# Optimization experiments

Measured on AMD Instinct MI355X. Metric: run time of the kernel, lower is better.

## Reference

```python
import jax, jax.numpy as jnp
import numpy as np

N_NODES = 128
B = 2048
N = B * N_NODES          # 262144 total nodes
E_PER = 512
E = B * E_PER            # 1048576 edges
H = 64                   # hidden_dim == embedding_dim
EPS = 1e-5


def _layernorm(x, g, b):
    m = x.mean(-1, keepdims=True)
    v = ((x - m) ** 2).mean(-1, keepdims=True)
    return (x - m) * jax.lax.rsqrt(v + EPS) * g + b


def setup_inputs() -> dict:
    key = jax.random.key(0)
    ks = jax.random.split(key, 16)
    node_feature = jax.random.randint(ks[0], (N,), 0, N_NODES, dtype=jnp.int32)
    # edges stay within each graph's node block
    offs = (jnp.arange(E, dtype=jnp.int32) // E_PER) * N_NODES
    src = offs + jax.random.randint(ks[1], (E,), 0, N_NODES, dtype=jnp.int32)
    dst = offs + jax.random.randint(ks[2], (E,), 0, N_NODES, dtype=jnp.int32)
    edge_index = jnp.stack([src, dst], axis=1)          # [E, 2]
    batch_ptr = jnp.arange(B + 1, dtype=jnp.int32) * N_NODES
    s = 0.1
    f32 = jnp.float32
    return {
        'node_feature': node_feature,
        'edge_index': edge_index,
        'batch_ptr': batch_ptr,
        'emb': jax.random.normal(ks[3], (N_NODES, H), f32),
        'gcn_w': jax.random.normal(ks[4], (H, H), f32) * s,
        'gcn_b': jnp.zeros((H,), f32),
        'lin1_w': jax.random.normal(ks[5], (H, H), f32) * s,
        'lin1_b': jnp.zeros((H,), f32),
        'lin2_w': jax.random.normal(ks[6], (H, H), f32) * s,
        'lin2_b': jnp.zeros((H,), f32),
        'ln_g': jnp.ones((H,), f32),
        'ln_b': jnp.zeros((H,), f32),
        'ex_w1': jax.random.normal(ks[7], (H, H), f32) * s,
        'ex_b1': jnp.zeros((H,), f32),
        'ex_ln_g': jnp.ones((H,), f32),
        'ex_ln_b': jnp.zeros((H,), f32),
        'ex_w2': jax.random.normal(ks[8], (H, 1), f32) * s,
        'ex_b2': jnp.zeros((1,), f32),
    }


def _forward(node_feature, edge_index, batch_ptr, emb, gcn_w, gcn_b,
             lin1_w, lin1_b, lin2_w, lin2_b, ln_g, ln_b,
             ex_w1, ex_b1, ex_ln_g, ex_ln_b, ex_w2, ex_b2):
    x = emb[node_feature]                                # [N, H] embedding lookup
    # --- GCNConv (PyG gcn_norm: self-loops + symmetric normalization) ---
    loops = jnp.arange(N, dtype=edge_index.dtype)
    src = jnp.concatenate([edge_index[:, 0], loops])
    dst = jnp.concatenate([edge_index[:, 1], loops])
    deg = jax.ops.segment_sum(jnp.ones_like(dst, dtype=x.dtype), dst, N)
    dinv = jnp.where(deg > 0, jax.lax.rsqrt(deg), 0.0)
    norm = dinv[src] * dinv[dst]                         # [E+N]
    h = x @ gcn_w                                        # linear (no bias)
    h = jax.ops.segment_sum(norm[:, None] * h[src], dst, N) + gcn_b
    # --- Linear -> ReLU -> Linear, residual, LayerNorm ---
    h = jnp.maximum(h @ lin1_w + lin1_b, 0.0) @ lin2_w + lin2_b
    ef = _layernorm(h + x, ln_g, ln_b)                   # [N, H]
    # --- cumsum-based group mean over batch_ptr segments ---
    cs = jnp.concatenate([jnp.zeros((1, H), ef.dtype), jnp.cumsum(ef, axis=0)], 0)
    size = (batch_ptr[1:] - batch_ptr[:-1]).astype(ef.dtype)
    means = (cs[batch_ptr[1:]] - cs[batch_ptr[:-1]]) / size[:, None]   # [B, H]
    # --- exit MLP: Linear -> LayerNorm -> ReLU -> Linear ---
    exit_action = jnp.maximum(_layernorm(means @ ex_w1 + ex_b1, ex_ln_g, ex_ln_b), 0.0) @ ex_w2 + ex_b2  # [B, 1]
    # --- pairwise edge logits + triu/tril gather (directed) ---
    efb = ef.reshape(B, N_NODES, H)
    scores = jnp.einsum('bnf,bmf->bnm', efb, efb) / jnp.sqrt(jnp.asarray(H, ef.dtype))
    iu0, iu1 = np.triu_indices(N_NODES, 1)
    il0, il1 = np.tril_indices(N_NODES, -1)
    i0 = jnp.asarray(np.concatenate([iu0, il0]))
    i1 = jnp.asarray(np.concatenate([iu1, il1]))
    edge_actions = scores[:, i0, i1]                     # [B, n^2 - n]
    return jnp.concatenate([edge_actions, exit_action], axis=-1)


def reference(node_feature, edge_index, batch_ptr, emb, gcn_w, gcn_b,
              lin1_w, lin1_b, lin2_w, lin2_b, ln_g, ln_b,
              ex_w1, ex_b1, ex_ln_g, ex_ln_b, ex_w2, ex_b2):
    return _forward(node_feature, edge_index, batch_ptr, emb, gcn_w, gcn_b,
                    lin1_w, lin1_b, lin2_w, lin2_b, ln_g, ln_b,
                    ex_w1, ex_b1, ex_ln_g, ex_ln_b, ex_w2, ex_b2)
```

## Files before the change

kernel.cpp:

```cpp
#include <hip/hip_runtime.h>

typedef __bf16 bf16_t;
typedef __bf16 bf16x8 __attribute__((ext_vector_type(8)));
typedef float  f32x4  __attribute__((ext_vector_type(4)));

#define LDR 72

__device__ __forceinline__ float bflo(unsigned u){ return __uint_as_float(u << 16); }
__device__ __forceinline__ float bfhi(unsigned u){ return __uint_as_float(u & 0xffff0000u); }

#define WS_MAP_OFF 24576

__global__ void prep_kernel(const float* __restrict__ emb,
                            const float* __restrict__ gcn_w,
                            const float* __restrict__ lin1_w,
                            const float* __restrict__ lin2_w,
                            bf16_t* __restrict__ ws)
{
    int t = blockIdx.x * 256 + threadIdx.x;
    bf16_t* emb_bf = ws;
    bf16_t* hw_bf  = ws + 8192;
    bf16_t* w1T    = ws + 16384;
    bf16_t* w2T    = ws + 20480;

    emb_bf[t] = (bf16_t)emb[t];
    int i = t >> 6, j = t & 63;
    float s = 0.f;
    #pragma unroll 8
    for (int k = 0; k < 64; ++k) s += emb[i*64 + k] * gcn_w[k*64 + j];
    hw_bf[t] = (bf16_t)s;
    if (t < 4096){
        int jj = t >> 6, kk = t & 63;
        w1T[t] = (bf16_t)lin1_w[kk*64 + jj];
        w2T[t] = (bf16_t)lin2_w[kk*64 + jj];
    }

    if (blockIdx.x == 0){
        __shared__ bf16_t pA[16*32];
        __shared__ bf16_t pB[16*32];
        int tid = threadIdx.x;
        for (int c = tid; c < 512; c += 256){
            int r = c >> 5, k = c & 31;
            pA[c] = (bf16_t)((k == 0) ? (float)r : ((k == 1) ? 1.f : 0.f));
            pB[c] = (bf16_t)((k == 0) ? 1.f : ((k == 1) ? (float)(128*r) : 0.f));
        }
        __syncthreads();
        if (tid < 64){
            int l15 = tid & 15, lg = tid >> 4;
            bf16x8 a  = *reinterpret_cast<const bf16x8*>(&pA[l15*32 + lg*8]);
            bf16x8 bb = *reinterpret_cast<const bf16x8*>(&pB[l15*32 + lg*8]);
            f32x4 acc = (f32x4){0.f,0.f,0.f,0.f};
            acc = __builtin_amdgcn_mfma_f32_16x16x32_bf16(a, bb, acc, 0, 0, 0);
            int* map = (int*)(ws + WS_MAP_OFF);
            #pragma unroll
            for (int r = 0; r < 4; ++r){
                int iv = (int)(acc[r] + 0.5f);
                map[tid*4 + r] = (iv & 127) | ((iv >> 7) << 8);
            }
        }
    }
}

__global__ __launch_bounds__(256, 3) void fused_kernel(
    const int*   __restrict__ node_feature,
    const int*   __restrict__ edge_index,
    const float* __restrict__ gcn_b,
    const float* __restrict__ lin1_b,
    const float* __restrict__ lin2_b,
    const float* __restrict__ ln_g,
    const float* __restrict__ ln_b,
    const float* __restrict__ ex_w1,
    const float* __restrict__ ex_b1,
    const float* __restrict__ ex_ln_g,
    const float* __restrict__ ex_ln_b,
    const float* __restrict__ ex_w2,
    const float* __restrict__ ex_b2,
    const bf16_t* __restrict__ ws,
    float* __restrict__ out)
{
    __shared__ __align__(16) bf16_t bufB[128*LDR];
    __shared__ __align__(16) bf16_t bufC[128*LDR];
    __shared__ unsigned short s_edge[512];
    __shared__ unsigned char  s_adj[512];
    __shared__ int   s_cnt[128];
    __shared__ int   s_start[128];
    __shared__ int   s_cur[128];
    __shared__ float s_dinv[128];
    __shared__ int   s_nf[128];
    __shared__ float s_b[320];
    __shared__ float s_pm[256];
    __shared__ float s_means[64];

    const int tid  = threadIdx.x;
    const int b    = blockIdx.x;
    const int wid  = tid >> 6;
    const int lane = tid & 63;
    const int l15  = lane & 15;
    const int lg   = lane >> 4;
    const long obase = (long)b * 16257;

    const bf16_t* emb_bf = ws;
    const bf16_t* hw_bf  = ws + 8192;
    const bf16_t* w1T    = ws + 16384;
    const bf16_t* w2T    = ws + 20480;

    int mi[4], mj[4];
    {
        const int* map = (const int*)(ws + WS_MAP_OFF);
        #pragma unroll
        for (int r = 0; r < 4; ++r){
            int m = map[lane*4 + r];
            mi[r] = m & 255; mj[r] = m >> 8;
        }
    }

    if (tid < 128){ s_nf[tid] = node_feature[b*128 + tid]; s_cnt[tid] = 0; }
    else if (tid < 192){
        int j = tid - 128;
        s_b[j]       = gcn_b[j];
        s_b[64 + j]  = lin1_b[j];
        s_b[128 + j] = lin2_b[j];
        s_b[192 + j] = ln_g[j];
        s_b[256 + j] = ln_b[j];
    }
    __syncthreads();

    {
        const int2* ei = reinterpret_cast<const int2*>(edge_index) + b*512;
        #pragma unroll
        for (int e = tid; e < 512; e += 256){
            int2 sd = ei[e];
            int s = sd.x & 127, d = sd.y & 127;
            s_edge[e] = (unsigned short)((s << 8) | d);
            atomicAdd(&s_cnt[d], 1);
        }
    }
    #pragma unroll
    for (int c = tid; c < 1024; c += 256){
        int row = c >> 3, ch = c & 7;
        int nf = s_nf[row];
        uint4 vh = reinterpret_cast<const uint4*>(hw_bf + nf*64)[ch];
        reinterpret_cast<uint4*>(&bufB[row*LDR])[ch] = vh;
    }
    __syncthreads();

    if (tid < 128) s_dinv[tid] = rsqrtf((float)(s_cnt[tid] + 1));
    if (tid < 64){
        int a0 = s_cnt[2*tid], a1 = s_cnt[2*tid+1];
        int s = a0 + a1;
        #pragma unroll
        for (int d = 1; d < 64; d <<= 1){
            int v = __shfl_up(s, d);
            if (lane >= d) s += v;
        }
        int excl = s - (a0 + a1);
        s_start[2*tid]   = excl;      s_cur[2*tid]   = excl;
        s_start[2*tid+1] = excl + a0; s_cur[2*tid+1] = excl + a0;
    }
    __syncthreads();
    #pragma unroll
    for (int e = tid; e < 512; e += 256){
        unsigned short sd = s_edge[e];
        int s = sd >> 8, d = sd & 255;
        int pos = atomicAdd(&s_cur[d], 1);
        s_adj[pos] = (unsigned char)s;
    }
    __syncthreads();

    {
        const int n  = tid >> 1;
        const int f0 = (tid & 1) << 5;
        float inner[32];
        #pragma unroll
        for (int f = 0; f < 32; ++f) inner[f] = 0.f;
        const float dn = s_dinv[n];
        {
            const uint4* hv = reinterpret_cast<const uint4*>(&bufB[n*LDR + f0]);
            #pragma unroll
            for (int q = 0; q < 4; ++q){
                uint4 v = hv[q];
                inner[q*8+0] += dn * bflo(v.x); inner[q*8+1] += dn * bfhi(v.x);
                inner[q*8+2] += dn * bflo(v.y); inner[q*8+3] += dn * bfhi(v.y);
                inner[q*8+4] += dn * bflo(v.z); inner[q*8+5] += dn * bfhi(v.z);
                inner[q*8+6] += dn * bflo(v.w); inner[q*8+7] += dn * bfhi(v.w);
            }
        }
        const int st = s_start[n], cn = s_cnt[n];
        for (int k = 0; k < cn; ++k){
            int src = s_adj[st + k];
            float w = s_dinv[src];
            const uint4* hv = reinterpret_cast<const uint4*>(&bufB[src*LDR + f0]);
            #pragma unroll
            for (int q = 0; q < 4; ++q){
                uint4 v = hv[q];
                inner[q*8+0] += w * bflo(v.x); inner[q*8+1] += w * bfhi(v.x);
                inner[q*8+2] += w * bflo(v.y); inner[q*8+3] += w * bfhi(v.y);
                inner[q*8+4] += w * bflo(v.z); inner[q*8+5] += w * bfhi(v.z);
                inner[q*8+6] += w * bflo(v.w); inner[q*8+7] += w * bfhi(v.w);
            }
        }
        #pragma unroll
        for (int f = 0; f < 32; ++f)
            bufC[n*LDR + f0 + f] = (bf16_t)(dn * inner[f] + s_b[f0 + f]);
    }
    __syncthreads();

    {
        bf16x8 af[2][2];
        #pragma unroll
        for (int fm = 0; fm < 2; ++fm)
            #pragma unroll
            for (int kk = 0; kk < 2; ++kk)
                af[fm][kk] = *reinterpret_cast<const bf16x8*>(
                    &bufC[(wid*32 + fm*16 + l15)*LDR + kk*32 + lg*8]);
        f32x4 acc[2][4];
        #pragma unroll
        for (int fm = 0; fm < 2; ++fm)
            #pragma unroll
            for (int fn = 0; fn < 4; ++fn)
                acc[fm][fn] = (f32x4){0.f,0.f,0.f,0.f};
        #pragma unroll
        for (int fn = 0; fn < 4; ++fn){
            #pragma unroll
            for (int kk = 0; kk < 2; ++kk){
                bf16x8 bfr = *reinterpret_cast<const bf16x8*>(
                    &w1T[(fn*16 + l15)*64 + kk*32 + lg*8]);
                #pragma unroll
                for (int fm = 0; fm < 2; ++fm)
                    acc[fm][fn] = __builtin_amdgcn_mfma_f32_16x16x32_bf16(
                        af[fm][kk], bfr, acc[fm][fn], 0, 0, 0);
            }
        }
        #pragma unroll
        for (int fm = 0; fm < 2; ++fm)
            #pragma unroll
            for (int fn = 0; fn < 4; ++fn)
                #pragma unroll
                for (int r = 0; r < 4; ++r){
                    int row = wid*32 + fm*16 + mi[r];
                    int col = fn*16 + mj[r];
                    float v = acc[fm][fn][r] + s_b[64 + col];
                    bufB[row*LDR + col] = (bf16_t)fmaxf(v, 0.f);
                }
    }
    __syncthreads();

    {
        bf16x8 af[2][2];
        #pragma unroll
        for (int fm = 0; fm < 2; ++fm)
            #pragma unroll
            for (int kk = 0; kk < 2; ++kk)
                af[fm][kk] = *reinterpret_cast<const bf16x8*>(
                    &bufB[(wid*32 + fm*16 + l15)*LDR + kk*32 + lg*8]);
        f32x4 acc[2][4];
        #pragma unroll
        for (int fm = 0; fm < 2; ++fm)
            #pragma unroll
            for (int fn = 0; fn < 4; ++fn)
                acc[fm][fn] = (f32x4){0.f,0.f,0.f,0.f};
        #pragma unroll
        for (int fn = 0; fn < 4; ++fn){
            #pragma unroll
            for (int kk = 0; kk < 2; ++kk){
                bf16x8 bfr = *reinterpret_cast<const bf16x8*>(
                    &w2T[(fn*16 + l15)*64 + kk*32 + lg*8]);
                #pragma unroll
                for (int fm = 0; fm < 2; ++fm)
                    acc[fm][fn] = __builtin_amdgcn_mfma_f32_16x16x32_bf16(
                        af[fm][kk], bfr, acc[fm][fn], 0, 0, 0);
            }
        }
        #pragma unroll
        for (int fm = 0; fm < 2; ++fm)
            #pragma unroll
            for (int fn = 0; fn < 4; ++fn)
                #pragma unroll
                for (int r = 0; r < 4; ++r){
                    int row = wid*32 + fm*16 + mi[r];
                    int col = fn*16 + mj[r];
                    bufC[row*LDR + col] = (bf16_t)(acc[fm][fn][r] + s_b[128 + col]);
                }
    }
    __syncthreads();

    {
        const int n  = tid >> 1;
        const int f0 = (tid & 1) << 5;
        const bf16x8* xp = reinterpret_cast<const bf16x8*>(&emb_bf[s_nf[n]*64 + f0]);
        float vv[32];
        float p1 = 0.f, p2 = 0.f;
        const bf16x8* rp = reinterpret_cast<const bf16x8*>(&bufC[n*LDR + f0]);
        #pragma unroll
        for (int q = 0; q < 4; ++q){
            bf16x8 v8 = rp[q];
            bf16x8 x8 = xp[q];
            #pragma unroll
            for (int e = 0; e < 8; ++e){
                float f = (float)v8[e] + (float)x8[e];
                vv[q*8+e] = f; p1 += f; p2 += f*f;
            }
        }
        p1 += __shfl_xor(p1, 1);
        p2 += __shfl_xor(p2, 1);
        float mean = p1 * 0.015625f;
        float var  = p2 * 0.015625f - mean*mean;
        float rstd = rsqrtf(var + 1e-5f);
        #pragma unroll
        for (int j = 0; j < 32; ++j)
            bufC[n*LDR + f0 + j] =
                (bf16_t)((vv[j] - mean) * rstd * s_b[192 + f0 + j] + s_b[256 + f0 + j]);
    }
    __syncthreads();

    {
        int col = tid & 63, q = tid >> 6;
        float s = 0.f;
        #pragma unroll 8
        for (int r = q*32; r < q*32 + 32; ++r)
            s += (float)bufC[r*LDR + col];
        s_pm[q*64 + col] = s;
    }
    __syncthreads();
    if (tid < 64)
        s_means[tid] = (s_pm[tid] + s_pm[64+tid] + s_pm[128+tid] + s_pm[192+tid]) * 0.0078125f;
    __syncthreads();

    if (tid < 64){
        float a = ex_b1[lane];
        #pragma unroll 8
        for (int k = 0; k < 64; ++k)
            a += s_means[k] * ex_w1[k*64 + lane];
        float p1 = a, p2 = a*a;
        #pragma unroll
        for (int m = 1; m < 64; m <<= 1){ p1 += __shfl_xor(p1, m); p2 += __shfl_xor(p2, m); }
        float mean = p1 * 0.015625f;
        float var  = p2 * 0.015625f - mean*mean;
        float u = (a - mean) * rsqrtf(var + 1e-5f) * ex_ln_g[lane] + ex_ln_b[lane];
        u = fmaxf(u, 0.f);
        float prod = u * ex_w2[lane];
        #pragma unroll
        for (int m = 1; m < 64; m <<= 1) prod += __shfl_xor(prod, m);
        if (lane == 0) out[obase + 16256] = prod + ex_b2[0];
    }

    {
        bf16x8 af[2][2];
        #pragma unroll
        for (int fm = 0; fm < 2; ++fm)
            #pragma unroll
            for (int kk = 0; kk < 2; ++kk)
                af[fm][kk] = *reinterpret_cast<const bf16x8*>(
                    &bufC[(wid*32 + fm*16 + l15)*LDR + kk*32 + lg*8]);
        f32x4 acc[2][8];
        #pragma unroll
        for (int fm = 0; fm < 2; ++fm)
            #pragma unroll
            for (int fn = 0; fn < 8; ++fn)
                acc[fm][fn] = (f32x4){0.f,0.f,0.f,0.f};
        #pragma unroll
        for (int fn = 0; fn < 8; ++fn){
            #pragma unroll
            for (int kk = 0; kk < 2; ++kk){
                bf16x8 bfr = *reinterpret_cast<const bf16x8*>(
                    &bufC[(fn*16 + l15)*LDR + kk*32 + lg*8]);
                #pragma unroll
                for (int fm = 0; fm < 2; ++fm)
                    acc[fm][fn] = __builtin_amdgcn_mfma_f32_16x16x32_bf16(
                        af[fm][kk], bfr, acc[fm][fn], 0, 0, 0);
            }
        }
        float* ob = out + obase;
        #pragma unroll
        for (int fm = 0; fm < 2; ++fm){
            #pragma unroll
            for (int fn = 0; fn < 8; ++fn){
                #pragma unroll
                for (int r = 0; r < 4; ++r){
                    int i = wid*32 + fm*16 + mi[r];
                    int j = fn*16 + mj[r];
                    if (i != j){
                        float v = acc[fm][fn][r] * 0.125f;
                        int p = (i < j) ? (i*127 - ((i*(i-1)) >> 1) + j - i - 1)
                                        : (8128 + ((i*(i-1)) >> 1) + j);
                        ob[p] = v;
                    }
                }
            }
        }
    }
}

extern "C" void kernel_launch(void* const* d_in, const int* in_sizes, int n_in,
                              void* d_out, int out_size, void* d_ws, size_t ws_size,
                              hipStream_t stream)
{
    const int*   node_feature = (const int*)  d_in[0];
    const int*   edge_index   = (const int*)  d_in[1];
    const float* emb     = (const float*)d_in[3];
    const float* gcn_w   = (const float*)d_in[4];
    const float* gcn_b   = (const float*)d_in[5];
    const float* lin1_w  = (const float*)d_in[6];
    const float* lin1_b  = (const float*)d_in[7];
    const float* lin2_w  = (const float*)d_in[8];
    const float* lin2_b  = (const float*)d_in[9];
    const float* ln_g    = (const float*)d_in[10];
    const float* ln_b    = (const float*)d_in[11];
    const float* ex_w1   = (const float*)d_in[12];
    const float* ex_b1   = (const float*)d_in[13];
    const float* ex_ln_g = (const float*)d_in[14];
    const float* ex_ln_b = (const float*)d_in[15];
    const float* ex_w2   = (const float*)d_in[16];
    const float* ex_b2   = (const float*)d_in[17];
    bf16_t* ws  = (bf16_t*)d_ws;
    float*  out = (float*)d_out;

    prep_kernel<<<32, 256, 0, stream>>>(emb, gcn_w, lin1_w, lin2_w, ws);
    fused_kernel<<<2048, 256, 0, stream>>>(node_feature, edge_index,
        gcn_b, lin1_b, lin2_b, ln_g, ln_b,
        ex_w1, ex_b1, ex_ln_g, ex_ln_b, ex_w2, ex_b2,
        ws, out);
}
```

Before: 70.77 us.

## Double block threads to 512 and alias shared scratch into one pool

Raises the fused kernel block size from 256 to 512 threads, so each wave now owns 16 rows instead of 32 in every MFMA stage and four threads share a node in the aggregation and layernorm stages. Shared scratch arrays are overlaid in a single pool and the separate degree-count array is dropped, with counts derived from prefix-start differences. This is meant to add latency hiding and shrink per-thread register and LDS footprint. In exchange, each B fragment is reused across fewer MFMAs and there are more waves per barrier.

After: 80.35 us. 1.14x slower.

```diff
diff --git a/kernel.cpp b/kernel.cpp
--- a/kernel.cpp
+++ b/kernel.cpp
@@ -61,7 +61,7 @@
     }
 }
 
-__global__ __launch_bounds__(256, 3) void fused_kernel(
+__global__ __launch_bounds__(512, 6) void fused_kernel(
     const int*   __restrict__ node_feature,
     const int*   __restrict__ edge_index,
     const float* __restrict__ gcn_b,
@@ -80,16 +80,16 @@
 {
     __shared__ __align__(16) bf16_t bufB[128*LDR];
     __shared__ __align__(16) bf16_t bufC[128*LDR];
-    __shared__ unsigned short s_edge[512];
-    __shared__ unsigned char  s_adj[512];
-    __shared__ int   s_cnt[128];
-    __shared__ int   s_start[128];
-    __shared__ int   s_cur[128];
-    __shared__ float s_dinv[128];
+    __shared__ __align__(16) unsigned char pool[2112];
+    __shared__ float s_b[320];
     __shared__ int   s_nf[128];
-    __shared__ float s_b[320];
-    __shared__ float s_pm[256];
-    __shared__ float s_means[64];
+
+    unsigned char* s_adj   = pool;
+    int*           s_start = (int*)(pool + 512);
+    int*           s_cur   = (int*)(pool + 1040);
+    float*         s_dinv  = (float*)(pool + 1552);
+    float*         s_pm    = (float*)pool;
+    float*         s_means = (float*)(pool + 1024);
 
     const int tid  = threadIdx.x;
     const int b    = blockIdx.x;
@@ -114,7 +114,9 @@
         }
     }
 
-    if (tid < 128){ s_nf[tid] = node_feature[b*128 + tid]; s_cnt[tid] = 0; }
+    const int2* ei = reinterpret_cast<const int2*>(edge_index) + b*512;
+
+    if (tid < 128){ s_nf[tid] = node_feature[b*128 + tid]; s_cur[tid] = 0; }
     else if (tid < 192){
         int j = tid - 128;
         s_b[j]       = gcn_b[j];
@@ -126,27 +128,21 @@
     __syncthreads();
 
     {
-        const int2* ei = reinterpret_cast<const int2*>(edge_index) + b*512;
-        #pragma unroll
-        for (int e = tid; e < 512; e += 256){
-            int2 sd = ei[e];
-            int s = sd.x & 127, d = sd.y & 127;
-            s_edge[e] = (unsigned short)((s << 8) | d);
-            atomicAdd(&s_cnt[d], 1);
-        }
+        int2 sd = ei[tid];
+        atomicAdd(&s_cur[sd.y & 127], 1);
     }
     #pragma unroll
-    for (int c = tid; c < 1024; c += 256){
+    for (int c = tid; c < 1024; c += 512){
         int row = c >> 3, ch = c & 7;
-        int nf = s_nf[row];
-        uint4 vh = reinterpret_cast<const uint4*>(hw_bf + nf*64)[ch];
+        uint4 vh = reinterpret_cast<const uint4*>(hw_bf + s_nf[row]*64)[ch];
         reinterpret_cast<uint4*>(&bufB[row*LDR])[ch] = vh;
     }
     __syncthreads();
 
-    if (tid < 128) s_dinv[tid] = rsqrtf((float)(s_cnt[tid] + 1));
     if (tid < 64){
-        int a0 = s_cnt[2*tid], a1 = s_cnt[2*tid+1];
+        int a0 = s_cur[2*tid], a1 = s_cur[2*tid+1];
+        s_dinv[2*tid]   = rsqrtf((float)(a0 + 1));
+        s_dinv[2*tid+1] = rsqrtf((float)(a1 + 1));
         int s = a0 + a1;
         #pragma unroll
         for (int d = 1; d < 64; d <<= 1){
@@ -154,30 +150,32 @@
             if (lane >= d) s += v;
         }
         int excl = s - (a0 + a1);
-        s_start[2*tid]   = excl;      s_cur[2*tid]   = excl;
-        s_start[2*tid+1] = excl + a0; s_cur[2*tid+1] = excl + a0;
-    }
-    __syncthreads();
-    #pragma unroll
-    for (int e = tid; e < 512; e += 256){
-        unsigned short sd = s_edge[e];
-        int s = sd >> 8, d = sd & 255;
-        int pos = atomicAdd(&s_cur[d], 1);
-        s_adj[pos] = (unsigned char)s;
-    }
-    __syncthreads();
-
-    {
-        const int n  = tid >> 1;
-        const int f0 = (tid & 1) << 5;
-        float inner[32];
-        #pragma unroll
-        for (int f = 0; f < 32; ++f) inner[f] = 0.f;
+        s_start[2*tid]   = excl;
+        s_start[2*tid+1] = excl + a0;
+        if (tid == 63) s_start[128] = 512;
+        s_cur[2*tid]   = excl;
+        s_cur[2*tid+1] = excl + a0;
+    }
+    __syncthreads();
+
+    {
+        int2 sd = ei[tid];
+        int pos = atomicAdd(&s_cur[sd.y & 127], 1);
+        s_adj[pos] = (unsigned char)(sd.x & 127);
+    }
+    __syncthreads();
+
+    {
+        const int n  = tid >> 2;
+        const int f0 = (tid & 3) << 4;
+        float inner[16];
+        #pragma unroll
+        for (int f = 0; f < 16; ++f) inner[f] = 0.f;
         const float dn = s_dinv[n];
         {
             const uint4* hv = reinterpret_cast<const uint4*>(&bufB[n*LDR + f0]);
             #pragma unroll
-            for (int q = 0; q < 4; ++q){
+            for (int q = 0; q < 2; ++q){
                 uint4 v = hv[q];
                 inner[q*8+0] += dn * bflo(v.x); inner[q*8+1] += dn * bfhi(v.x);
                 inner[q*8+2] += dn * bflo(v.y); inner[q*8+3] += dn * bfhi(v.y);
@@ -185,13 +183,13 @@
                 inner[q*8+6] += dn * bflo(v.w); inner[q*8+7] += dn * bfhi(v.w);
             }
         }
-        const int st = s_start[n], cn = s_cnt[n];
+        const int st = s_start[n], cn = s_start[n+1] - st;
         for (int k = 0; k < cn; ++k){
             int src = s_adj[st + k];
             float w = s_dinv[src];
             const uint4* hv = reinterpret_cast<const uint4*>(&bufB[src*LDR + f0]);
             #pragma unroll
-            for (int q = 0; q < 4; ++q){
+            for (int q = 0; q < 2; ++q){
                 uint4 v = hv[q];
                 inner[q*8+0] += w * bflo(v.x); inner[q*8+1] += w * bfhi(v.x);
                 inner[q*8+2] += w * bflo(v.y); inner[q*8+3] += w * bfhi(v.y);
@@ -200,99 +198,76 @@
             }
         }
         #pragma unroll
-        for (int f = 0; f < 32; ++f)
+        for (int f = 0; f < 16; ++f)
             bufC[n*LDR + f0 + f] = (bf16_t)(dn * inner[f] + s_b[f0 + f]);
     }
     __syncthreads();
 
     {
-        bf16x8 af[2][2];
-        #pragma unroll
-        for (int fm = 0; fm < 2; ++fm)
-            #pragma unroll
-            for (int kk = 0; kk < 2; ++kk)
-                af[fm][kk] = *reinterpret_cast<const bf16x8*>(
-                    &bufC[(wid*32 + fm*16 + l15)*LDR + kk*32 + lg*8]);
-        f32x4 acc[2][4];
-        #pragma unroll
-        for (int fm = 0; fm < 2; ++fm)
-            #pragma unroll
-            for (int fn = 0; fn < 4; ++fn)
-                acc[fm][fn] = (f32x4){0.f,0.f,0.f,0.f};
-        #pragma unroll
-        for (int fn = 0; fn < 4; ++fn){
+        bf16x8 af[2];
+        #pragma unroll
+        for (int kk = 0; kk < 2; ++kk)
+            af[kk] = *reinterpret_cast<const bf16x8*>(
+                &bufC[(wid*16 + l15)*LDR + kk*32 + lg*8]);
+        f32x4 acc[4];
+        #pragma unroll
+        for (int fn = 0; fn < 4; ++fn) acc[fn] = (f32x4){0.f,0.f,0.f,0.f};
+        #pragma unroll
+        for (int fn = 0; fn < 4; ++fn)
             #pragma unroll
             for (int kk = 0; kk < 2; ++kk){
                 bf16x8 bfr = *reinterpret_cast<const bf16x8*>(
                     &w1T[(fn*16 + l15)*64 + kk*32 + lg*8]);
-                #pragma unroll
-                for (int fm = 0; fm < 2; ++fm)
-                    acc[fm][fn] = __builtin_amdgcn_mfma_f32_16x16x32_bf16(
-                        af[fm][kk], bfr, acc[fm][fn], 0, 0, 0);
-            }
-        }
-        #pragma unroll
-        for (int fm = 0; fm < 2; ++fm)
-            #pragma unroll
-            for (int fn = 0; fn < 4; ++fn)
-                #pragma unroll
-                for (int r = 0; r < 4; ++r){
-                    int row = wid*32 + fm*16 + mi[r];
-                    int col = fn*16 + mj[r];
-                    float v = acc[fm][fn][r] + s_b[64 + col];
-                    bufB[row*LDR + col] = (bf16_t)fmaxf(v, 0.f);
-                }
-    }
-    __syncthreads();
-
-    {
-        bf16x8 af[2][2];
-        #pragma unroll
-        for (int fm = 0; fm < 2; ++fm)
-            #pragma unroll
-            for (int kk = 0; kk < 2; ++kk)
-                af[fm][kk] = *reinterpret_cast<const bf16x8*>(
-                    &bufB[(wid*32 + fm*16 + l15)*LDR + kk*32 + lg*8]);
-        f32x4 acc[2][4];
-        #pragma unroll
-        for (int fm = 0; fm < 2; ++fm)
-            #pragma unroll
-            for (int fn = 0; fn < 4; ++fn)
-                acc[fm][fn] = (f32x4){0.f,0.f,0.f,0.f};
-        #pragma unroll
-        for (int fn = 0; fn < 4; ++fn){
+                acc[fn] = __builtin_amdgcn_mfma_f32_16x16x32_bf16(af[kk], bfr, acc[fn], 0, 0, 0);
+            }
+        #pragma unroll
+        for (int fn = 0; fn < 4; ++fn)
+            #pragma unroll
+            for (int r = 0; r < 4; ++r){
+                int row = wid*16 + mi[r];
+                int col = fn*16 + mj[r];
+                bufB[row*LDR + col] = (bf16_t)fmaxf(acc[fn][r] + s_b[64 + col], 0.f);
+            }
+    }
+    __syncthreads();
+
+    {
+        bf16x8 af[2];
+        #pragma unroll
+        for (int kk = 0; kk < 2; ++kk)
+            af[kk] = *reinterpret_cast<const bf16x8*>(
+                &bufB[(wid*16 + l15)*LDR + kk*32 + lg*8]);
+        f32x4 acc[4];
+        #pragma unroll
+        for (int fn = 0; fn < 4; ++fn) acc[fn] = (f32x4){0.f,0.f,0.f,0.f};
+        #pragma unroll
+        for (int fn = 0; fn < 4; ++fn)
             #pragma unroll
             for (int kk = 0; kk < 2; ++kk){
                 bf16x8 bfr = *reinterpret_cast<const bf16x8*>(
                     &w2T[(fn*16 + l15)*64 + kk*32 + lg*8]);
-                #pragma unroll
-                for (int fm = 0; fm < 2; ++fm)
-                    acc[fm][fn] = __builtin_amdgcn_mfma_f32_16x16x32_bf16(
-                        af[fm][kk], bfr, acc[fm][fn], 0, 0, 0);
-            }
-        }
-        #pragma unroll
-        for (int fm = 0; fm < 2; ++fm)
-            #pragma unroll
-            for (int fn = 0; fn < 4; ++fn)
-                #pragma unroll
-                for (int r = 0; r < 4; ++r){
-                    int row = wid*32 + fm*16 + mi[r];
-                    int col = fn*16 + mj[r];
-                    bufC[row*LDR + col] = (bf16_t)(acc[fm][fn][r] + s_b[128 + col]);
-                }
-    }
-    __syncthreads();
-
-    {
-        const int n  = tid >> 1;
-        const int f0 = (tid & 1) << 5;
+                acc[fn] = __builtin_amdgcn_mfma_f32_16x16x32_bf16(af[kk], bfr, acc[fn], 0, 0, 0);
+            }
+        #pragma unroll
+        for (int fn = 0; fn < 4; ++fn)
+            #pragma unroll
+            for (int r = 0; r < 4; ++r){
+                int row = wid*16 + mi[r];
+                int col = fn*16 + mj[r];
+                bufC[row*LDR + col] = (bf16_t)(acc[fn][r] + s_b[128 + col]);
+            }
+    }
+    __syncthreads();
+
+    {
+        const int n  = tid >> 2;
+        const int f0 = (tid & 3) << 4;
         const bf16x8* xp = reinterpret_cast<const bf16x8*>(&emb_bf[s_nf[n]*64 + f0]);
-        float vv[32];
+        const bf16x8* rp = reinterpret_cast<const bf16x8*>(&bufC[n*LDR + f0]);
+        float vv[16];
         float p1 = 0.f, p2 = 0.f;
-        const bf16x8* rp = reinterpret_cast<const bf16x8*>(&bufC[n*LDR + f0]);
-        #pragma unroll
-        for (int q = 0; q < 4; ++q){
+        #pragma unroll
+        for (int q = 0; q < 2; ++q){
             bf16x8 v8 = rp[q];
             bf16x8 x8 = xp[q];
             #pragma unroll
@@ -301,19 +276,19 @@
                 vv[q*8+e] = f; p1 += f; p2 += f*f;
             }
         }
-        p1 += __shfl_xor(p1, 1);
-        p2 += __shfl_xor(p2, 1);
+        p1 += __shfl_xor(p1, 1); p2 += __shfl_xor(p2, 1);
+        p1 += __shfl_xor(p1, 2); p2 += __shfl_xor(p2, 2);
         float mean = p1 * 0.015625f;
         float var  = p2 * 0.015625f - mean*mean;
         float rstd = rsqrtf(var + 1e-5f);
         #pragma unroll
-        for (int j = 0; j < 32; ++j)
+        for (int j = 0; j < 16; ++j)
             bufC[n*LDR + f0 + j] =
                 (bf16_t)((vv[j] - mean) * rstd * s_b[192 + f0 + j] + s_b[256 + f0 + j]);
     }
     __syncthreads();
 
-    {
+    if (tid < 256){
         int col = tid & 63, q = tid >> 6;
         float s = 0.f;
         #pragma unroll 8
@@ -345,46 +320,34 @@
     }
 
     {
-        bf16x8 af[2][2];
-        #pragma unroll
-        for (int fm = 0; fm < 2; ++fm)
-            #pragma unroll
-            for (int kk = 0; kk < 2; ++kk)
-                af[fm][kk] = *reinterpret_cast<const bf16x8*>(
-                    &bufC[(wid*32 + fm*16 + l15)*LDR + kk*32 + lg*8]);
-        f32x4 acc[2][8];
-        #pragma unroll
-        for (int fm = 0; fm < 2; ++fm)
-            #pragma unroll
-            for (int fn = 0; fn < 8; ++fn)
-                acc[fm][fn] = (f32x4){0.f,0.f,0.f,0.f};
-        #pragma unroll
-        for (int fn = 0; fn < 8; ++fn){
+        bf16x8 af[2];
+        #pragma unroll
+        for (int kk = 0; kk < 2; ++kk)
+            af[kk] = *reinterpret_cast<const bf16x8*>(
+                &bufC[(wid*16 + l15)*LDR + kk*32 + lg*8]);
+        f32x4 acc[8];
+        #pragma unroll
+        for (int fn = 0; fn < 8; ++fn) acc[fn] = (f32x4){0.f,0.f,0.f,0.f};
+        #pragma unroll
+        for (int fn = 0; fn < 8; ++fn)
             #pragma unroll
             for (int kk = 0; kk < 2; ++kk){
                 bf16x8 bfr = *reinterpret_cast<const bf16x8*>(
                     &bufC[(fn*16 + l15)*LDR + kk*32 + lg*8]);
-                #pragma unroll
-                for (int fm = 0; fm < 2; ++fm)
-                    acc[fm][fn] = __builtin_amdgcn_mfma_f32_16x16x32_bf16(
-                        af[fm][kk], bfr, acc[fm][fn], 0, 0, 0);
-            }
-        }
+                acc[fn] = __builtin_amdgcn_mfma_f32_16x16x32_bf16(af[kk], bfr, acc[fn], 0, 0, 0);
+            }
         float* ob = out + obase;
         #pragma unroll
-        for (int fm = 0; fm < 2; ++fm){
-            #pragma unroll
-            for (int fn = 0; fn < 8; ++fn){
-                #pragma unroll
-                for (int r = 0; r < 4; ++r){
-                    int i = wid*32 + fm*16 + mi[r];
-                    int j = fn*16 + mj[r];
-                    if (i != j){
-                        float v = acc[fm][fn][r] * 0.125f;
-                        int p = (i < j) ? (i*127 - ((i*(i-1)) >> 1) + j - i - 1)
-                                        : (8128 + ((i*(i-1)) >> 1) + j);
-                        ob[p] = v;
-                    }
+        for (int fn = 0; fn < 8; ++fn){
+            #pragma unroll
+            for (int r = 0; r < 4; ++r){
+                int i = wid*16 + mi[r];
+                int j = fn*16 + mj[r];
+                if (i != j){
+                    float v = acc[fn][r] * 0.125f;
+                    int p = (i < j) ? (i*127 - ((i*(i-1)) >> 1) + j - i - 1)
+                                    : (8128 + ((i*(i-1)) >> 1) + j);
+                    ob[p] = v;
                 }
             }
         }
@@ -416,7 +379,7 @@
     float*  out = (float*)d_out;
 
     prep_kernel<<<32, 256, 0, stream>>>(emb, gcn_w, lin1_w, lin2_w, ws);
-    fused_kernel<<<2048, 256, 0, stream>>>(node_feature, edge_index,
+    fused_kernel<<<2048, 512, 0, stream>>>(node_feature, edge_index,
         gcn_b, lin1_b, lin2_b, ln_g, ln_b,
         ex_w1, ex_b1, ex_ln_g, ex_ln_b, ex_w2, ex_b2,
         ws, out);
```

## Vectorize score stores via MFMA layout probe, shrink shared memory for higher occupancy

Applied to the files above, without the earlier changes.

The prep kernel now checks whether the MFMA accumulator layout puts four consecutive columns in one lane and records a flag. When the flag is set, the fused kernel writes pairwise scores as 16-byte vector stores instead of scalar stores, falling back to scalar writes near the diagonal. Shared memory is shrunk by aliasing scratch arrays into a pool, storing node features as bytes, dropping the bias staging array (biases are read from global) and keeping edges in registers. The launch bound is raised from 3 to 4 blocks per CU. Reading biases from global adds load traffic, and the extra occupancy constrains register use.

Measured after the change: 71.86 us. Within noise of the previous version (+1.5%).

```diff
diff --git a/kernel.cpp b/kernel.cpp
--- a/kernel.cpp
+++ b/kernel.cpp
@@ -3,6 +3,7 @@
 typedef __bf16 bf16_t;
 typedef __bf16 bf16x8 __attribute__((ext_vector_type(8)));
 typedef float  f32x4  __attribute__((ext_vector_type(4)));
+typedef f32x4  f32x4u __attribute__((aligned(4)));
 
 #define LDR 72
 
@@ -52,16 +53,23 @@
             f32x4 acc = (f32x4){0.f,0.f,0.f,0.f};
             acc = __builtin_amdgcn_mfma_f32_16x16x32_bf16(a, bb, acc, 0, 0, 0);
             int* map = (int*)(ws + WS_MAP_OFF);
+            int mi[4], mj[4];
             #pragma unroll
             for (int r = 0; r < 4; ++r){
                 int iv = (int)(acc[r] + 0.5f);
-                map[tid*4 + r] = (iv & 127) | ((iv >> 7) << 8);
-            }
+                mi[r] = iv & 127; mj[r] = iv >> 7;
+                map[tid*4 + r] = mi[r] | (mj[r] << 8);
+            }
+            bool ok = (mi[0]==mi[1] && mi[1]==mi[2] && mi[2]==mi[3] &&
+                       mj[1]==mj[0]+1 && mj[2]==mj[0]+2 && mj[3]==mj[0]+3 &&
+                       (mj[0] & 3) == 0);
+            unsigned long long all = __ballot(ok);
+            if (tid == 0) map[256] = (all == ~0ull) ? 1 : 0;
         }
     }
 }
 
-__global__ __launch_bounds__(256, 3) void fused_kernel(
+__global__ __launch_bounds__(256, 4) void fused_kernel(
     const int*   __restrict__ node_feature,
     const int*   __restrict__ edge_index,
     const float* __restrict__ gcn_b,
@@ -80,16 +88,15 @@
 {
     __shared__ __align__(16) bf16_t bufB[128*LDR];
     __shared__ __align__(16) bf16_t bufC[128*LDR];
-    __shared__ unsigned short s_edge[512];
-    __shared__ unsigned char  s_adj[512];
-    __shared__ int   s_cnt[128];
-    __shared__ int   s_start[128];
-    __shared__ int   s_cur[128];
-    __shared__ float s_dinv[128];
-    __shared__ int   s_nf[128];
-    __shared__ float s_b[320];
-    __shared__ float s_pm[256];
-    __shared__ float s_means[64];
+    __shared__ __align__(8)  unsigned char pool[2176];
+    __shared__ unsigned char s_nf8[128];
+
+    unsigned char* s_adj   = pool;
+    int*           s_start = (int*)(pool + 512);
+    int*           s_cur   = (int*)(pool + 1040);
+    float*         s_dinv  = (float*)(pool + 1552);
+    float*         s_pm    = (float*)pool;
+    float*         s_means = (float*)(pool + 1024);
 
     const int tid  = threadIdx.x;
     const int b    = blockIdx.x;
@@ -104,7 +111,7 @@
     const bf16_t* w1T    = ws + 16384;
     const bf16_t* w2T    = ws + 20480;
 
-    int mi[4], mj[4];
+    int mi[4], mj[4], vflag;
     {
         const int* map = (const int*)(ws + WS_MAP_OFF);
         #pragma unroll
@@ -112,41 +119,31 @@
             int m = map[lane*4 + r];
             mi[r] = m & 255; mj[r] = m >> 8;
         }
-    }
-
-    if (tid < 128){ s_nf[tid] = node_feature[b*128 + tid]; s_cnt[tid] = 0; }
-    else if (tid < 192){
-        int j = tid - 128;
-        s_b[j]       = gcn_b[j];
-        s_b[64 + j]  = lin1_b[j];
-        s_b[128 + j] = lin2_b[j];
-        s_b[192 + j] = ln_g[j];
-        s_b[256 + j] = ln_b[j];
-    }
-    __syncthreads();
-
-    {
-        const int2* ei = reinterpret_cast<const int2*>(edge_index) + b*512;
-        #pragma unroll
-        for (int e = tid; e < 512; e += 256){
-            int2 sd = ei[e];
-            int s = sd.x & 127, d = sd.y & 127;
-            s_edge[e] = (unsigned short)((s << 8) | d);
-            atomicAdd(&s_cnt[d], 1);
-        }
-    }
+        vflag = map[256];
+    }
+
+    const int2* ei = reinterpret_cast<const int2*>(edge_index) + b*512;
+    int2 e0 = ei[tid];
+    int2 e1 = ei[tid + 256];
+
+    if (tid < 128) s_nf8[tid] = (unsigned char)node_feature[b*128 + tid];
+    else           s_cur[tid - 128] = 0;
+    __syncthreads();
+
+    atomicAdd(&s_cur[e0.y & 127], 1);
+    atomicAdd(&s_cur[e1.y & 127], 1);
     #pragma unroll
     for (int c = tid; c < 1024; c += 256){
         int row = c >> 3, ch = c & 7;
-        int nf = s_nf[row];
-        uint4 vh = reinterpret_cast<const uint4*>(hw_bf + nf*64)[ch];
+        uint4 vh = reinterpret_cast<const uint4*>(hw_bf + (int)s_nf8[row]*64)[ch];
         reinterpret_cast<uint4*>(&bufB[row*LDR])[ch] = vh;
     }
     __syncthreads();
 
-    if (tid < 128) s_dinv[tid] = rsqrtf((float)(s_cnt[tid] + 1));
     if (tid < 64){
-        int a0 = s_cnt[2*tid], a1 = s_cnt[2*tid+1];
+        int a0 = s_cur[2*tid], a1 = s_cur[2*tid+1];
+        s_dinv[2*tid]   = rsqrtf((float)(a0 + 1));
+        s_dinv[2*tid+1] = rsqrtf((float)(a1 + 1));
         int s = a0 + a1;
         #pragma unroll
         for (int d = 1; d < 64; d <<= 1){
@@ -154,16 +151,19 @@
             if (lane >= d) s += v;
         }
         int excl = s - (a0 + a1);
-        s_start[2*tid]   = excl;      s_cur[2*tid]   = excl;
-        s_start[2*tid+1] = excl + a0; s_cur[2*tid+1] = excl + a0;
-    }
-    __syncthreads();
-    #pragma unroll
-    for (int e = tid; e < 512; e += 256){
-        unsigned short sd = s_edge[e];
-        int s = sd >> 8, d = sd & 255;
-        int pos = atomicAdd(&s_cur[d], 1);
-        s_adj[pos] = (unsigned char)s;
+        s_start[2*tid]   = excl;
+        s_start[2*tid+1] = excl + a0;
+        if (tid == 63) s_start[128] = 512;
+        s_cur[2*tid]   = excl;
+        s_cur[2*tid+1] = excl + a0;
+    }
+    __syncthreads();
+
+    {
+        int pos0 = atomicAdd(&s_cur[e0.y & 127], 1);
+        s_adj[pos0] = (unsigned char)(e0.x & 127);
+        int pos1 = atomicAdd(&s_cur[e1.y & 127], 1);
+        s_adj[pos1] = (unsigned char)(e1.x & 127);
     }
     __syncthreads();
 
@@ -185,7 +185,7 @@
                 inner[q*8+6] += dn * bflo(v.w); inner[q*8+7] += dn * bfhi(v.w);
             }
         }
-        const int st = s_start[n], cn = s_cnt[n];
+        const int st = s_start[n], cn = s_start[n+1] - st;
         for (int k = 0; k < cn; ++k){
             int src = s_adj[st + k];
             float w = s_dinv[src];
@@ -199,9 +199,10 @@
                 inner[q*8+6] += w * bflo(v.w); inner[q*8+7] += w * bfhi(v.w);
             }
         }
+        const float* gb = gcn_b + f0;
         #pragma unroll
         for (int f = 0; f < 32; ++f)
-            bufC[n*LDR + f0 + f] = (bf16_t)(dn * inner[f] + s_b[f0 + f]);
+            bufC[n*LDR + f0 + f] = (bf16_t)(dn * inner[f] + gb[f]);
     }
     __syncthreads();
 
@@ -220,7 +221,7 @@
             for (int fn = 0; fn < 4; ++fn)
                 acc[fm][fn] = (f32x4){0.f,0.f,0.f,0.f};
         #pragma unroll
-        for (int fn = 0; fn < 4; ++fn){
+        for (int fn = 0; fn < 4; ++fn)
             #pragma unroll
             for (int kk = 0; kk < 2; ++kk){
                 bf16x8 bfr = *reinterpret_cast<const bf16x8*>(
@@ -230,7 +231,6 @@
                     acc[fm][fn] = __builtin_amdgcn_mfma_f32_16x16x32_bf16(
                         af[fm][kk], bfr, acc[fm][fn], 0, 0, 0);
             }
-        }
         #pragma unroll
         for (int fm = 0; fm < 2; ++fm)
             #pragma unroll
@@ -239,8 +239,7 @@
                 for (int r = 0; r < 4; ++r){
                     int row = wid*32 + fm*16 + mi[r];
                     int col = fn*16 + mj[r];
-                    float v = acc[fm][fn][r] + s_b[64 + col];
-                    bufB[row*LDR + col] = (bf16_t)fmaxf(v, 0.f);
+                    bufB[row*LDR + col] = (bf16_t)fmaxf(acc[fm][fn][r] + lin1_b[col], 0.f);
                 }
     }
     __syncthreads();
@@ -260,7 +259,7 @@
             for (int fn = 0; fn < 4; ++fn)
                 acc[fm][fn] = (f32x4){0.f,0.f,0.f,0.f};
         #pragma unroll
-        for (int fn = 0; fn < 4; ++fn){
+        for (int fn = 0; fn < 4; ++fn)
             #pragma unroll
             for (int kk = 0; kk < 2; ++kk){
                 bf16x8 bfr = *reinterpret_cast<const bf16x8*>(
@@ -270,7 +269,6 @@
                     acc[fm][fn] = __builtin_amdgcn_mfma_f32_16x16x32_bf16(
                         af[fm][kk], bfr, acc[fm][fn], 0, 0, 0);
             }
-        }
         #pragma unroll
         for (int fm = 0; fm < 2; ++fm)
             #pragma unroll
@@ -279,7 +277,7 @@
                 for (int r = 0; r < 4; ++r){
                     int row = wid*32 + fm*16 + mi[r];
                     int col = fn*16 + mj[r];
-                    bufC[row*LDR + col] = (bf16_t)(acc[fm][fn][r] + s_b[128 + col]);
+                    bufC[row*LDR + col] = (bf16_t)(acc[fm][fn][r] + lin2_b[col]);
                 }
     }
     __syncthreads();
@@ -287,10 +285,10 @@
     {
         const int n  = tid >> 1;
         const int f0 = (tid & 1) << 5;
-        const bf16x8* xp = reinterpret_cast<const bf16x8*>(&emb_bf[s_nf[n]*64 + f0]);
+        const bf16x8* xp = reinterpret_cast<const bf16x8*>(&emb_bf[(int)s_nf8[n]*64 + f0]);
+        const bf16x8* rp = reinterpret_cast<const bf16x8*>(&bufC[n*LDR + f0]);
         float vv[32];
         float p1 = 0.f, p2 = 0.f;
-        const bf16x8* rp = reinterpret_cast<const bf16x8*>(&bufC[n*LDR + f0]);
         #pragma unroll
         for (int q = 0; q < 4; ++q){
             bf16x8 v8 = rp[q];
@@ -306,10 +304,11 @@
         float mean = p1 * 0.015625f;
         float var  = p2 * 0.015625f - mean*mean;
         float rstd = rsqrtf(var + 1e-5f);
+        const float* lg_ = ln_g + f0;
+        const float* lb_ = ln_b + f0;
         #pragma unroll
         for (int j = 0; j < 32; ++j)
-            bufC[n*LDR + f0 + j] =
-                (bf16_t)((vv[j] - mean) * rstd * s_b[192 + f0 + j] + s_b[256 + f0 + j]);
+            bufC[n*LDR + f0 + j] = (bf16_t)((vv[j] - mean) * rstd * lg_[j] + lb_[j]);
     }
     __syncthreads();
 
@@ -359,7 +358,7 @@
             for (int fn = 0; fn < 8; ++fn)
                 acc[fm][fn] = (f32x4){0.f,0.f,0.f,0.f};
         #pragma unroll
-        for (int fn = 0; fn < 8; ++fn){
+        for (int fn = 0; fn < 8; ++fn)
             #pragma unroll
             for (int kk = 0; kk < 2; ++kk){
                 bf16x8 bfr = *reinterpret_cast<const bf16x8*>(
@@ -369,21 +368,47 @@
                     acc[fm][fn] = __builtin_amdgcn_mfma_f32_16x16x32_bf16(
                         af[fm][kk], bfr, acc[fm][fn], 0, 0, 0);
             }
-        }
         float* ob = out + obase;
-        #pragma unroll
-        for (int fm = 0; fm < 2; ++fm){
-            #pragma unroll
-            for (int fn = 0; fn < 8; ++fn){
-                #pragma unroll
-                for (int r = 0; r < 4; ++r){
-                    int i = wid*32 + fm*16 + mi[r];
-                    int j = fn*16 + mj[r];
-                    if (i != j){
-                        float v = acc[fm][fn][r] * 0.125f;
-                        int p = (i < j) ? (i*127 - ((i*(i-1)) >> 1) + j - i - 1)
-                                        : (8128 + ((i*(i-1)) >> 1) + j);
-                        ob[p] = v;
+        if (vflag){
+            #pragma unroll
+            for (int fm = 0; fm < 2; ++fm){
+                int i = wid*32 + fm*16 + mi[0];
+                int tri = (i*(i-1)) >> 1;
+                int c_tu = i*127 - tri - i - 1;
+                int c_tl = 8128 + tri;
+                #pragma unroll
+                for (int fn = 0; fn < 8; ++fn){
+                    int jb = fn*16 + mj[0];
+                    f32x4 w = acc[fm][fn] * 0.125f;
+                    if (i < jb){
+                        *reinterpret_cast<f32x4u*>(ob + c_tu + jb) = w;
+                    } else if (i > jb + 3){
+                        *reinterpret_cast<f32x4u*>(ob + c_tl + jb) = w;
+                    } else {
+                        #pragma unroll
+                        for (int r = 0; r < 4; ++r){
+                            int j = jb + r;
+                            if (i != j)
+                                ob[(i < j) ? (c_tu + j) : (c_tl + j)] = w[r];
+                        }
+                    }
+                }
+            }
+        } else {
+            #pragma unroll
+            for (int fm = 0; fm < 2; ++fm){
+                #pragma unroll
+                for (int fn = 0; fn < 8; ++fn){
+                    #pragma unroll
+                    for (int r = 0; r < 4; ++r){
+                        int i = wid*32 + fm*16 + mi[r];
+                        int j = fn*16 + mj[r];
+                        if (i != j){
+                            float v = acc[fm][fn][r] * 0.125f;
+                            int p = (i < j) ? (i*127 - ((i*(i-1)) >> 1) + j - i - 1)
+                                            : (8128 + ((i*(i-1)) >> 1) + j);
+                            ob[p] = v;
+                        }
                     }
                 }
             }
```
